# Performance work log

Measured on AMD Instinct MI355X. Metric: run time of the kernel, lower is better.

## Reference

```python
import jax, jax.numpy as jnp
import numpy as np

N_HEAD = 8
D_MODEL = 1024   # also the sequence length L (the code requires L == d_model)
D_K = 256
D_V = 256
D_TRANS = 256
B = 32
KS = 13
PAD = 6
LN_EPS = 1e-3
TEMPER = float(np.sqrt(D_MODEL))


def conv1d(x, w, b):
    # x: (B, Cin, L), w: (Cout, Cin, K) torch layout, 'same' padding 6
    y = jax.lax.conv_general_dilated(
        x, w, window_strides=(1,), padding=[(PAD, PAD)],
        dimension_numbers=('NCH', 'OIH', 'NCH'))
    return y + b[None, :, None]


def setup_inputs() -> dict:
    key = jax.random.key(0)
    ks = jax.random.split(key, 16)
    n = lambda i, shape, s=1.0: jax.random.normal(ks[i], shape, jnp.float32) * s
    return {
        'q': n(0, (B, D_K, D_MODEL)),
        'k': n(1, (B, D_K, D_MODEL)),
        'v': n(2, (B, D_V, D_MODEL)),
        'cq_w': n(3, (D_TRANS, D_K, KS), 0.02), 'cq_b': jnp.zeros((D_TRANS,), jnp.float32),
        'ck_w': n(4, (D_TRANS, D_K, KS), 0.02), 'ck_b': jnp.zeros((D_TRANS,), jnp.float32),
        'cv_w': n(5, (D_TRANS, D_V, KS), 0.02), 'cv_b': jnp.zeros((D_TRANS,), jnp.float32),
        'w_qs': n(6, (N_HEAD, D_MODEL, D_TRANS), 0.02),
        'w_ks': n(7, (N_HEAD, D_MODEL, D_TRANS), 0.02),
        'w_vs': n(8, (N_HEAD, D_MODEL, D_TRANS), 0.02),
        'proj_w': n(9, (D_MODEL, N_HEAD * D_TRANS), 0.02),
        'proj_b': jnp.zeros((D_MODEL,), jnp.float32),
        'fc_w': n(10, (D_V, D_TRANS, KS), 0.02), 'fc_b': jnp.zeros((D_V,), jnp.float32),
        'ln_a': jnp.ones((D_MODEL,), jnp.float32),
        'ln_b': jnp.zeros((D_MODEL,), jnp.float32),
    }


def reference(q, k, v, cq_w, cq_b, ck_w, ck_b, cv_w, cv_b,
              w_qs, w_ks, w_vs, proj_w, proj_b, fc_w, fc_b, ln_a, ln_b):
    # Conv1d QKV "projections": (B, d_k, L) -> (B, d_trans, L)
    q_b = conv1d(q, cq_w, cq_b)
    k_b = conv1d(k, ck_w, ck_b)
    v_b = conv1d(v, cv_w, cv_b)

    # Per-head projection along the L (==d_model) axis:
    # torch: (H, B*d_trans, L) bmm (H, L, d_trans) -> (H*B, d_trans, d_trans)
    q_s = jnp.einsum('btl,hld->hbtd', q_b, w_qs)  # (H, B, Dt, Dt)
    k_s = jnp.einsum('btl,hld->hbtd', k_b, w_ks)
    v_s = jnp.einsum('btl,hld->hbtd', v_b, w_vs)

    # Scaled dot-product attention over the d_trans axis (eval mode: dropout off)
    scores = jnp.einsum('hbqd,hbkd->hbqk', q_s, k_s) / TEMPER
    attn = jax.nn.softmax(scores, axis=-1)
    out = jnp.einsum('hbqk,hbkd->hbqd', attn, v_s)  # (H, B, Dt, Dt)

    # torch: split heads along batch dim, concat along last -> (B, Dt, H*Dt)
    outputs = out.transpose(1, 2, 0, 3).reshape(B, D_TRANS, N_HEAD * D_TRANS)
    outputs = outputs @ proj_w.T + proj_b            # (B, Dt, d_model)
    outputs = conv1d(outputs, fc_w, fc_b)            # (B, d_v, d_model)

    # Custom LayerNorm over last axis with unbiased std and eps added to sigma
    z = outputs + q
    mu = jnp.mean(z, axis=-1, keepdims=True)
    sigma = jnp.std(z, axis=-1, ddof=1, keepdims=True)
    output = (z - mu) / (sigma + LN_EPS) * ln_a + ln_b

    attns = attn.reshape(N_HEAD * B, D_TRANS, D_TRANS)
    return output, attns
```

## Files before the change

### kernel.cpp

```cpp
#include <hip/hip_runtime.h>

typedef unsigned short u16;
typedef __attribute__((ext_vector_type(8))) short short8;
typedef __attribute__((ext_vector_type(4))) float f32x4;

__device__ __forceinline__ float bf2f(u16 x) {
  unsigned u = ((unsigned)x) << 16;
  return __builtin_bit_cast(float, u);
}
__device__ __forceinline__ u16 f2bf(float x) {
  unsigned u = __builtin_bit_cast(unsigned, x);
  u += 0x7fffu + ((u >> 16) & 1u);
  return (u16)(u >> 16);
}

__device__ __forceinline__ void gl2lds16(const u16* g, u16* l) {
  __builtin_amdgcn_global_load_lds(
      (const __attribute__((address_space(1))) unsigned*)g,
      (__attribute__((address_space(3))) unsigned*)l, 16, 0, 0);
}

__global__ void detect_kernel(const void* ln_a, unsigned* flag) {
  if (threadIdx.x == 0 && blockIdx.x == 0)
    *flag = (*(const unsigned*)ln_a == 0x3F800000u) ? 1u : 0u;
}

#define GEMM_TILE(T, RB, DO_STAGE, SB, VMCNT, ENDBAR)                         \
  {                                                                           \
    const u16* ring_ = smem + (RB)*BUF;                                       \
    short8 af_[4], bq_[4];                                                    \
    _Pragma("unroll") for (int i_ = 0; i_ < 4; i_++)                          \
        af_[i_] = *(const short8*)(ring_ + offA[i_]);                         \
    _Pragma("unroll") for (int j_ = 0; j_ < 4; j_++)                          \
        bq_[j_] = *(const short8*)(ring_ + offB[j_]);                         \
    if (DO_STAGE) stage_tile((T) + AHEAD, (SB));                              \
    __builtin_amdgcn_s_barrier();                                             \
    asm volatile("s_waitcnt lgkmcnt(0)" ::: "memory");                        \
    __builtin_amdgcn_sched_barrier(0);                                        \
    __builtin_amdgcn_s_setprio(1);                                            \
    _Pragma("unroll") for (int i_ = 0; i_ < 4; i_++)                          \
        _Pragma("unroll") for (int j_ = 0; j_ < 4; j_++)                      \
            acc[i_][j_] = __builtin_amdgcn_mfma_f32_16x16x32_bf16(            \
                af_[i_], bq_[j_], acc[i_][j_], 0, 0, 0);                      \
    __builtin_amdgcn_s_setprio(0);                                            \
    if constexpr (WIDE) {                                                     \
      _Pragma("unroll") for (int i_ = 0; i_ < 4; i_++)                        \
          af_[i_] = *(const short8*)(ring_ + offA[4 + i_]);                   \
      asm volatile("s_waitcnt lgkmcnt(0)" ::: "memory");                      \
      __builtin_amdgcn_sched_barrier(0);                                      \
      __builtin_amdgcn_s_setprio(1);                                          \
      _Pragma("unroll") for (int i_ = 0; i_ < 4; i_++)                        \
          _Pragma("unroll") for (int j_ = 0; j_ < 4; j_++)                    \
              acc[4 + i_][j_] = __builtin_amdgcn_mfma_f32_16x16x32_bf16(      \
                  af_[i_], bq_[j_], acc[4 + i_][j_], 0, 0, 0);                \
      __builtin_amdgcn_s_setprio(0);                                          \
    }                                                                         \
    if ((VMCNT) == 6) asm volatile("s_waitcnt vmcnt(6)" ::: "memory");        \
    else if ((VMCNT) == 4) asm volatile("s_waitcnt vmcnt(4)" ::: "memory");   \
    else if ((VMCNT) == 3) asm volatile("s_waitcnt vmcnt(3)" ::: "memory");   \
    else if ((VMCNT) == 0) asm volatile("s_waitcnt vmcnt(0)" ::: "memory");   \
    if (ENDBAR) __builtin_amdgcn_s_barrier();                                 \
  }

template <typename OutT, bool WIDE>
__global__ __launch_bounds__(512, 2) void gemm_kernel(
    const u16* __restrict__ A, const u16* __restrict__ B, OutT* __restrict__ C,
    const u16* __restrict__ bias, int K, int lda, int ldb, int ldc,
    long a0, long a1, long a2, long b0, long b1, long b2,
    long c0, long c1, long c2, int biasMid, float alpha) {
  extern __shared__ u16 smem[];
  constexpr int BN = WIDE ? 256 : 128;
  constexpr int BUF = WIDE ? 16384 : 12288;
  constexpr int RING = WIDE ? 3 : 4;
  constexpr int AHEAD = RING - 1;
  constexpr int NCALL = WIDE ? 4 : 3;
  constexpr int MI = WIDE ? 8 : 4;

  const int tid = threadIdx.x;
  const int z = blockIdx.z;
  const int zlo = z & 31, zmid = (z >> 5) & 7, zhi = z >> 8;
  const u16* Ab = A + (long)zlo * a0 + (long)zmid * a1 + (long)zhi * a2;
  const u16* Bb = B + (long)zlo * b0 + (long)zmid * b1 + (long)zhi * b2;
  OutT* Cb = C + (long)zlo * c0 + (long)zmid * c1 + (long)zhi * c2;
  const int m0 = blockIdx.y * 256;
  const int n0 = blockIdx.x * BN;

  const int wave = tid >> 6;
  const int lane = tid & 63;

  const int lgrp = lane >> 3;
  const int slot = lane & 7;
  const u16* gsrc[NCALL];
  int ldsoff[NCALL];
#pragma unroll
  for (int c = 0; c < NCALL; c++) {
    const bool isA = (c < 2);
    const int L0 = (isA ? c : (c - 2)) * 64 + wave * 8;
    const int L = L0 + lgrp;
    const int ls = slot ^ (L & 7);
    const int row = 2 * L + (ls >> 2);
    const int blk = ls & 3;
    if (isA) {
      gsrc[c] = Ab + (long)(m0 + row) * lda + blk * 8;
      ldsoff[c] = L0 * 64;
    } else {
      gsrc[c] = Bb + (long)(n0 + row) * ldb + blk * 8;
      ldsoff[c] = 8192 + L0 * 64;
    }
  }

  auto stage_tile = [&](int t, int buf) {
    u16* dst = smem + buf * BUF;
    const long koff = (long)t * 32;
#pragma unroll
    for (int c = 0; c < NCALL; c++) gl2lds16(gsrc[c] + koff, dst + ldsoff[c]);
  };

  const int wm = WIDE ? ((wave >> 2) * 128) : ((wave >> 1) * 64);
  const int wn = WIDE ? ((wave & 3) * 64) : ((wave & 1) * 64);
  const int quad = lane >> 4;
  const int r = lane & 15;
  int offA[MI], offB[4];
#pragma unroll
  for (int i = 0; i < MI; i++) {
    const int rowA = wm + i * 16 + r;
    const int lnA = rowA >> 1;
    offA[i] = lnA * 64 + ((((rowA & 1) * 4 + quad) ^ (lnA & 7)) * 8);
  }
#pragma unroll
  for (int j = 0; j < 4; j++) {
    const int rowB = wn + j * 16 + r;
    const int lnB = rowB >> 1;
    offB[j] = 8192 + lnB * 64 + ((((rowB & 1) * 4 + quad) ^ (lnB & 7)) * 8);
  }

  f32x4 acc[MI][4] = {};
  const int nt = K >> 5;

#pragma unroll
  for (int i = 0; i < AHEAD; i++) stage_tile(i, i);
  if constexpr (WIDE)
    asm volatile("s_waitcnt vmcnt(4)" ::: "memory");
  else
    asm volatile("s_waitcnt vmcnt(6)" ::: "memory");
  __builtin_amdgcn_s_barrier();

  int t = 0, rbuf = 0, sbuf = AHEAD;
  for (; t < nt - AHEAD; ++t) {
    GEMM_TILE(t, rbuf, true, sbuf, (WIDE ? 4 : 6), true);
    rbuf = (rbuf + 1 == RING) ? 0 : rbuf + 1;
    sbuf = (sbuf + 1 == RING) ? 0 : sbuf + 1;
  }
  if constexpr (!WIDE) {
    GEMM_TILE(t, rbuf, false, 0, 3, true);
    ++t;
    rbuf = (rbuf + 1 == RING) ? 0 : rbuf + 1;
  }
  GEMM_TILE(t, rbuf, false, 0, 0, true);
  ++t;
  rbuf = (rbuf + 1 == RING) ? 0 : rbuf + 1;
  GEMM_TILE(t, rbuf, false, 0, -1, false);

  const u16* biasb = bias ? bias + (long)zmid * biasMid : nullptr;
#pragma unroll
  for (int i = 0; i < MI; i++) {
#pragma unroll
    for (int rr = 0; rr < 4; rr++) {
      const int mg = m0 + wm + i * 16 + quad * 4 + rr;
      const float bv = biasb ? bf2f(biasb[mg]) : 0.0f;
#pragma unroll
      for (int j = 0; j < 4; j++) {
        const int ng = n0 + wn + j * 16 + r;
        float val = acc[i][j][rr] * alpha + bv;
        if constexpr (__is_same(OutT, float))
          Cb[(long)mg * ldc + ng] = val;
        else
          Cb[(long)mg * ldc + ng] = f2bf(val);
      }
    }
  }
}

__global__ __launch_bounds__(256) void transpose_kernel(
    const void* __restrict__ i0, const void* __restrict__ i1,
    const void* __restrict__ i2, u16* __restrict__ out, int R, int C,
    long ostride, int ooff, int zdiv, const unsigned* __restrict__ flagp) {
  const bool f32 = *flagp != 0;
  __shared__ u16 t[64 * 68];
  const int z = blockIdx.z;
  const void* in = (z < zdiv) ? i0 : (z < 2 * zdiv) ? i1 : i2;
  const int zq = (z < zdiv) ? z : (z < 2 * zdiv) ? z - zdiv : z - 2 * zdiv;
  const long ibase = (long)zq * R * C;
  const int r0 = blockIdx.y * 64;
  const int c0 = blockIdx.x * 64;
  u16* ob = out + (long)z * ostride + ooff;
  const int tid = threadIdx.x;
#pragma unroll
  for (int i = 0; i < 4; i++) {
    const int vv = tid + i * 256;
    const int rr = vv >> 4;
    const int cc = (vv & 15) << 2;
    uint2 packed;
    if (f32) {
      const float4 fv = *(const float4*)((const float*)in + ibase +
                                         (long)(r0 + rr) * C + (c0 + cc));
      packed.x = (unsigned)f2bf(fv.x) | ((unsigned)f2bf(fv.y) << 16);
      packed.y = (unsigned)f2bf(fv.z) | ((unsigned)f2bf(fv.w) << 16);
    } else {
      packed = *(const uint2*)((const u16*)in + ibase + (long)(r0 + rr) * C +
                               (c0 + cc));
    }
    *(uint2*)(&t[rr * 68 + cc]) = packed;
  }
  __syncthreads();
#pragma unroll
  for (int i = 0; i < 4; i++) {
    const int vv = tid + i * 256;
    const int cc = vv >> 4;
    const int rr = (vv & 15) << 2;
    unsigned lo = (unsigned)t[rr * 68 + cc] | ((unsigned)t[(rr + 1) * 68 + cc] << 16);
    unsigned hi =
        (unsigned)t[(rr + 2) * 68 + cc] | ((unsigned)t[(rr + 3) * 68 + cc] << 16);
    uint2 val = {lo, hi};
    *(uint2*)(ob + (long)(c0 + cc) * R + (r0 + rr)) = val;
  }
}

__global__ __launch_bounds__(256) void pack_w_kernel(
    const void* __restrict__ w0, const void* __restrict__ w1,
    const void* __restrict__ w2, const void* __restrict__ w3,
    u16* __restrict__ out, const unsigned* __restrict__ flagp) {
  const bool f32 = *flagp != 0;
  const int y = blockIdx.y;
  const void* in = (y == 0) ? w0 : (y == 1) ? w1 : (y == 2) ? w2 : w3;
  u16* o = out + (long)y * 851968;
  const int t = blockIdx.x * 256 + threadIdx.x;
  const int co = t / 3328;
  const int rem = t - co * 3328;
  const int dk = rem >> 8;
  const int ci = rem & 255;
  const int src = co * 3328 + ci * 13 + dk;
  o[t] = f32 ? f2bf(((const float*)in)[src]) : ((const u16*)in)[src];
}

__global__ __launch_bounds__(256) void cvt_kernel(const void* __restrict__ in,
                                                  u16* __restrict__ out, long n,
                                                  const unsigned* __restrict__ flagp) {
  const bool f32 = *flagp != 0;
  const long i = ((long)blockIdx.x * 256 + threadIdx.x) * 8;
  if (i >= n) return;
  if (f32) {
    const float* p = (const float*)in + i;
    const float4 a = *(const float4*)p;
    const float4 b = *(const float4*)(p + 4);
    uint4 o;
    o.x = (unsigned)f2bf(a.x) | ((unsigned)f2bf(a.y) << 16);
    o.y = (unsigned)f2bf(a.z) | ((unsigned)f2bf(a.w) << 16);
    o.z = (unsigned)f2bf(b.x) | ((unsigned)f2bf(b.y) << 16);
    o.w = (unsigned)f2bf(b.z) | ((unsigned)f2bf(b.w) << 16);
    *(uint4*)(out + i) = o;
  } else {
    *(uint4*)(out + i) = *(const uint4*)((const u16*)in + i);
  }
}

__global__ __launch_bounds__(256) void bias_cvt_kernel(
    const void* __restrict__ s0, const void* __restrict__ s1,
    const void* __restrict__ s2, const void* __restrict__ s3,
    const void* __restrict__ s4, u16* __restrict__ out,
    const unsigned* __restrict__ flagp) {
  const bool f32 = *flagp != 0;
  const long i = threadIdx.x * 8;
  const void* src;
  long off;
  if (i < 256) { src = s0; off = i; }
  else if (i < 512) { src = s1; off = i - 256; }
  else if (i < 768) { src = s2; off = i - 512; }
  else if (i < 1024) { src = s3; off = i - 768; }
  else { src = s4; off = i - 1024; }
  if (f32) {
    const float* p = (const float*)src + off;
    const float4 a = *(const float4*)p;
    const float4 b = *(const float4*)(p + 4);
    uint4 o;
    o.x = (unsigned)f2bf(a.x) | ((unsigned)f2bf(a.y) << 16);
    o.y = (unsigned)f2bf(a.z) | ((unsigned)f2bf(a.w) << 16);
    o.z = (unsigned)f2bf(b.x) | ((unsigned)f2bf(b.y) << 16);
    o.w = (unsigned)f2bf(b.z) | ((unsigned)f2bf(b.w) << 16);
    *(uint4*)(out + i) = o;
  } else {
    *(uint4*)(out + i) = *(const uint4*)((const u16*)src + off);
  }
}

__global__ __launch_bounds__(256) void zeropad_kernel(u16* __restrict__ base,
                                                      long bstride, int nb) {
  const int t = blockIdx.x * 256 + threadIdx.x;
  if (t >= nb * 384) return;
  const int b = t / 384;
  const int rem = t - b * 384;
  const int rp = rem >> 5;
  const int col = (rem & 31) * 8;
  const int row = rp < 6 ? rp : 1024 + rp;
  uint4 zz = {0u, 0u, 0u, 0u};
  *(uint4*)(base + (long)b * bstride + row * 256 + col) = zz;
}

__global__ __launch_bounds__(256) void softmax_kernel(
    u16* __restrict__ sc, void* __restrict__ dout,
    const unsigned* __restrict__ flagp) {
  const bool f32 = *flagp != 0;
  const long row = (long)blockIdx.x * 4 + (threadIdx.x >> 6);
  const int lane = threadIdx.x & 63;
  const uint2 raw = *(const uint2*)(sc + row * 256 + lane * 4);
  float s0 = bf2f((u16)(raw.x & 0xffff)), s1 = bf2f((u16)(raw.x >> 16));
  float s2 = bf2f((u16)(raw.y & 0xffff)), s3 = bf2f((u16)(raw.y >> 16));
  float m = fmaxf(fmaxf(s0, s1), fmaxf(s2, s3));
  for (int o = 32; o > 0; o >>= 1) m = fmaxf(m, __shfl_xor(m, o, 64));
  float e0 = expf(s0 - m), e1 = expf(s1 - m), e2 = expf(s2 - m), e3 = expf(s3 - m);
  float sum = e0 + e1 + e2 + e3;
  for (int o = 32; o > 0; o >>= 1) sum += __shfl_xor(sum, o, 64);
  const float inv = 1.0f / sum;
  const float p0 = e0 * inv, p1 = e1 * inv, p2 = e2 * inv, p3 = e3 * inv;
  uint2 ov;
  ov.x = (unsigned)f2bf(p0) | ((unsigned)f2bf(p1) << 16);
  ov.y = (unsigned)f2bf(p2) | ((unsigned)f2bf(p3) << 16);
  *(uint2*)(sc + row * 256 + lane * 4) = ov;
  if (f32) {
    float4 o4 = {p0, p1, p2, p3};
    *(float4*)((float*)dout + 8388608 + row * 256 + lane * 4) = o4;
  } else {
    *(uint2*)((u16*)dout + 8388608 + row * 256 + lane * 4) = ov;
  }
}

__global__ __launch_bounds__(256) void ln_kernel(
    const float* __restrict__ fc, const void* __restrict__ qraw,
    const void* __restrict__ la, const void* __restrict__ lb,
    void* __restrict__ dout, const unsigned* __restrict__ flagp) {
  const bool f32 = *flagp != 0;
  __shared__ float red[4];
  const long row = blockIdx.x;
  const int tid = threadIdx.x;
  const int col = tid * 4;
  const float4 zf = *(const float4*)(fc + row * 1024 + col);
  float q0, q1, q2, q3;
  if (f32) {
    const float4 t = *(const float4*)((const float*)qraw + row * 1024 + col);
    q0 = t.x; q1 = t.y; q2 = t.z; q3 = t.w;
  } else {
    const uint2 qr = *(const uint2*)((const u16*)qraw + row * 1024 + col);
    q0 = bf2f((u16)(qr.x & 0xffff)); q1 = bf2f((u16)(qr.x >> 16));
    q2 = bf2f((u16)(qr.y & 0xffff)); q3 = bf2f((u16)(qr.y >> 16));
  }
  const float z0 = zf.x + q0, z1 = zf.y + q1, z2 = zf.z + q2, z3 = zf.w + q3;
  float s = z0 + z1 + z2 + z3;
  for (int o = 32; o > 0; o >>= 1) s += __shfl_xor(s, o, 64);
  if ((tid & 63) == 0) red[tid >> 6] = s;
  __syncthreads();
  const float mu = (red[0] + red[1] + red[2] + red[3]) * (1.0f / 1024.0f);
  __syncthreads();
  const float d0 = z0 - mu, d1 = z1 - mu, d2 = z2 - mu, d3 = z3 - mu;
  float ss = d0 * d0 + d1 * d1 + d2 * d2 + d3 * d3;
  for (int o = 32; o > 0; o >>= 1) ss += __shfl_xor(ss, o, 64);
  if ((tid & 63) == 0) red[tid >> 6] = ss;
  __syncthreads();
  const float var = (red[0] + red[1] + red[2] + red[3]) * (1.0f / 1023.0f);
  const float inv = 1.0f / (sqrtf(var) + 1e-3f);
  float a0, a1, a2, a3, b0, b1, b2, b3;
  if (f32) {
    const float4 ta = *(const float4*)((const float*)la + col);
    const float4 tb = *(const float4*)((const float*)lb + col);
    a0 = ta.x; a1 = ta.y; a2 = ta.z; a3 = ta.w;
    b0 = tb.x; b1 = tb.y; b2 = tb.z; b3 = tb.w;
  } else {
    const uint2 ta = *(const uint2*)((const u16*)la + col);
    const uint2 tb = *(const uint2*)((const u16*)lb + col);
    a0 = bf2f((u16)(ta.x & 0xffff)); a1 = bf2f((u16)(ta.x >> 16));
    a2 = bf2f((u16)(ta.y & 0xffff)); a3 = bf2f((u16)(ta.y >> 16));
    b0 = bf2f((u16)(tb.x & 0xffff)); b1 = bf2f((u16)(tb.x >> 16));
    b2 = bf2f((u16)(tb.y & 0xffff)); b3 = bf2f((u16)(tb.y >> 16));
  }
  const float o0 = d0 * inv * a0 + b0, o1 = d1 * inv * a1 + b1;
  const float o2v = d2 * inv * a2 + b2, o3 = d3 * inv * a3 + b3;
  if (f32) {
    float4 o4 = {o0, o1, o2v, o3};
    *(float4*)((float*)dout + row * 1024 + col) = o4;
  } else {
    uint2 o2;
    o2.x = (unsigned)f2bf(o0) | ((unsigned)f2bf(o1) << 16);
    o2.y = (unsigned)f2bf(o2v) | ((unsigned)f2bf(o3) << 16);
    *(uint2*)((u16*)dout + row * 1024 + col) = o2;
  }
}

enum : long {
  OWPQ = 0,
  OWPK = 851968,
  OWPV = 1703936,
  OWPFC = 2555904,
  OWQT = 3407872,
  OWKT = 5505024,
  OWVT = 7602176,
  OPW16 = 9699328,
  OBQKV = 11796480,
  OBFC = 11797248,
  OBPROJ = 11797504,
  OFLAG = 11798528,
  OQB = 11798536,
  OKB = 20187144,
  OVB = 28575752,
  OQS = 36964360,
  OKS = 53741576,
  OVST = 70518792,
  OXPAD = OQS,
  OSC = OQB,
  OOUTC = OQS,
  OPROJP = OKS,
  OFC = OVST,
};

extern "C" void kernel_launch(void* const* d_in, const int* in_sizes, int n_in,
                              void* d_out, int out_size, void* d_ws,
                              size_t ws_size, hipStream_t stream) {
  const void* q = d_in[0];
  const void* k = d_in[1];
  const void* v = d_in[2];
  const void* cq_w = d_in[3];
  const void* cq_b = d_in[4];
  const void* ck_w = d_in[5];
  const void* ck_b = d_in[6];
  const void* cv_w = d_in[7];
  const void* cv_b = d_in[8];
  const void* w_qs = d_in[9];
  const void* w_ks = d_in[10];
  const void* w_vs = d_in[11];
  const void* proj_w = d_in[12];
  const void* proj_b = d_in[13];
  const void* fc_w = d_in[14];
  const void* fc_b = d_in[15];
  const void* ln_a = d_in[16];
  const void* ln_b = d_in[17];

  u16* ws = (u16*)d_ws;
  unsigned* flag = (unsigned*)(ws + OFLAG);

  static int attr_done = 0;
  if (!attr_done) {
    hipFuncSetAttribute(reinterpret_cast<const void*>(&gemm_kernel<u16, true>),
                        hipFuncAttributeMaxDynamicSharedMemorySize, 98304);
    hipFuncSetAttribute(reinterpret_cast<const void*>(&gemm_kernel<u16, false>),
                        hipFuncAttributeMaxDynamicSharedMemorySize, 98304);
    hipFuncSetAttribute(reinterpret_cast<const void*>(&gemm_kernel<float, false>),
                        hipFuncAttributeMaxDynamicSharedMemorySize, 98304);
    attr_done = 1;
  }

  detect_kernel<<<1, 64, 0, stream>>>(ln_a, flag);

  pack_w_kernel<<<dim3(3328, 4), 256, 0, stream>>>(cq_w, ck_w, cv_w, fc_w,
                                                   ws + OWPQ, flag);
  transpose_kernel<<<dim3(4, 16, 24), 256, 0, stream>>>(
      w_qs, w_ks, w_vs, ws + OWQT, 1024, 256, 262144, 0, 8, flag);
  cvt_kernel<<<1024, 256, 0, stream>>>(proj_w, ws + OPW16, 2097152, flag);
  bias_cvt_kernel<<<1, 256, 0, stream>>>(cq_b, ck_b, cv_b, fc_b, proj_b,
                                         ws + OBQKV, flag);

  zeropad_kernel<<<144, 256, 0, stream>>>(ws + OXPAD, 265216, 96);
  transpose_kernel<<<dim3(16, 4, 96), 256, 0, stream>>>(
      q, k, v, ws + OXPAD, 256, 1024, 265216, 1536, 32, flag);

  gemm_kernel<u16, true><<<dim3(4, 1, 96), 512, 98304, stream>>>(
      ws + OWPQ, ws + OXPAD, ws + OQB, ws + OBQKV, 3328, 3328, 256, 1024,
      0, 851968, 0, 265216, 8486912, 0, 262144, 8388608, 0, 256, 1.0f);

  gemm_kernel<u16, true><<<dim3(1, 1, 512), 512, 98304, stream>>>(
      ws + OQB, ws + OWQT, ws + OQS, nullptr, 1024, 1024, 1024, 256,
      262144, 0, 8388608, 0, 262144, 2097152, 65536, 2097152, 16777216, 0, 1.0f);
  gemm_kernel<u16, true><<<dim3(1, 1, 256), 512, 98304, stream>>>(
      ws + OWVT, ws + OVB, ws + OVST, nullptr, 1024, 1024, 1024, 256,
      0, 262144, 0, 262144, 0, 0, 65536, 2097152, 0, 0, 1.0f);

  gemm_kernel<u16, true><<<dim3(1, 1, 256), 512, 98304, stream>>>(
      ws + OQS, ws + OKS, ws + OSC, nullptr, 256, 256, 256, 256,
      65536, 2097152, 0, 65536, 2097152, 0, 65536, 2097152, 0, 0, 0.03125f);

  softmax_kernel<<<16384, 256, 0, stream>>>(ws + OSC, d_out, flag);

  gemm_kernel<u16, true><<<dim3(1, 1, 256), 512, 98304, stream>>>(
      ws + OSC, ws + OVST, ws + OOUTC, nullptr, 256, 256, 256, 2048,
      65536, 2097152, 0, 65536, 2097152, 0, 524288, 256, 0, 0, 1.0f);

  zeropad_kernel<<<48, 256, 0, stream>>>(ws + OPROJP, 265216, 32);
  gemm_kernel<u16, false><<<dim3(2, 4, 32), 512, 98304, stream>>>(
      ws + OPW16, ws + OOUTC, ws + OPROJP + 1536, ws + OBPROJ, 2048, 2048, 2048,
      256, 0, 0, 0, 524288, 0, 0, 265216, 0, 0, 0, 1.0f);

  gemm_kernel<float, false><<<dim3(8, 1, 32), 512, 98304, stream>>>(
      ws + OWPFC, ws + OPROJP, (float*)(ws + OFC), ws + OBFC, 3328, 3328, 256,
      1024, 0, 0, 0, 265216, 0, 0, 262144, 0, 0, 0, 1.0f);

  ln_kernel<<<8192, 256, 0, stream>>>((const float*)(ws + OFC), q, ln_a, ln_b,
                                      d_out, flag);

  (void)in_sizes; (void)n_in; (void)out_size; (void)ws_size;
}
```

Measured before the change: 794.2 us.

## Restructure GEMM main loop into split-A register prefetch with three-buffer ring

Replaces the macro-based GEMM tile loop with a single loop that keeps a fixed three-buffer LDS ring, prefetching the next tile's A-low and B fragments into registers while MFMAs on the current half run. Each iteration uses one barrier plus staged lgkmcnt waits, so LDS reads overlap compute more finely. The conv QKV GEMM also switches from the wide 256-column tile to the narrow 128-column tile, doubling the grid to raise occupancy. Risks: more register pressure, a full vmcnt(0) wait every iteration, and the narrow variant now uses only 3 of its 4 ring buffers with a different vmcnt count.

```diff
diff --git a/kernel.cpp b/kernel.cpp
--- a/kernel.cpp
+++ b/kernel.cpp
@@ -24,43 +24,6 @@
   if (threadIdx.x == 0 && blockIdx.x == 0)
     *flag = (*(const unsigned*)ln_a == 0x3F800000u) ? 1u : 0u;
 }
-
-#define GEMM_TILE(T, RB, DO_STAGE, SB, VMCNT, ENDBAR)                         \
-  {                                                                           \
-    const u16* ring_ = smem + (RB)*BUF;                                       \
-    short8 af_[4], bq_[4];                                                    \
-    _Pragma("unroll") for (int i_ = 0; i_ < 4; i_++)                          \
-        af_[i_] = *(const short8*)(ring_ + offA[i_]);                         \
-    _Pragma("unroll") for (int j_ = 0; j_ < 4; j_++)                          \
-        bq_[j_] = *(const short8*)(ring_ + offB[j_]);                         \
-    if (DO_STAGE) stage_tile((T) + AHEAD, (SB));                              \
-    __builtin_amdgcn_s_barrier();                                             \
-    asm volatile("s_waitcnt lgkmcnt(0)" ::: "memory");                        \
-    __builtin_amdgcn_sched_barrier(0);                                        \
-    __builtin_amdgcn_s_setprio(1);                                            \
-    _Pragma("unroll") for (int i_ = 0; i_ < 4; i_++)                          \
-        _Pragma("unroll") for (int j_ = 0; j_ < 4; j_++)                      \
-            acc[i_][j_] = __builtin_amdgcn_mfma_f32_16x16x32_bf16(            \
-                af_[i_], bq_[j_], acc[i_][j_], 0, 0, 0);                      \
-    __builtin_amdgcn_s_setprio(0);                                            \
-    if constexpr (WIDE) {                                                     \
-      _Pragma("unroll") for (int i_ = 0; i_ < 4; i_++)                        \
-          af_[i_] = *(const short8*)(ring_ + offA[4 + i_]);                   \
-      asm volatile("s_waitcnt lgkmcnt(0)" ::: "memory");                      \
-      __builtin_amdgcn_sched_barrier(0);                                      \
-      __builtin_amdgcn_s_setprio(1);                                          \
-      _Pragma("unroll") for (int i_ = 0; i_ < 4; i_++)                        \
-          _Pragma("unroll") for (int j_ = 0; j_ < 4; j_++)                    \
-              acc[4 + i_][j_] = __builtin_amdgcn_mfma_f32_16x16x32_bf16(      \
-                  af_[i_], bq_[j_], acc[4 + i_][j_], 0, 0, 0);                \
-      __builtin_amdgcn_s_setprio(0);                                          \
-    }                                                                         \
-    if ((VMCNT) == 6) asm volatile("s_waitcnt vmcnt(6)" ::: "memory");        \
-    else if ((VMCNT) == 4) asm volatile("s_waitcnt vmcnt(4)" ::: "memory");   \
-    else if ((VMCNT) == 3) asm volatile("s_waitcnt vmcnt(3)" ::: "memory");   \
-    else if ((VMCNT) == 0) asm volatile("s_waitcnt vmcnt(0)" ::: "memory");   \
-    if (ENDBAR) __builtin_amdgcn_s_barrier();                                 \
-  }
 
 template <typename OutT, bool WIDE>
 __global__ __launch_bounds__(512, 2) void gemm_kernel(
@@ -71,10 +34,9 @@
   extern __shared__ u16 smem[];
   constexpr int BN = WIDE ? 256 : 128;
   constexpr int BUF = WIDE ? 16384 : 12288;
-  constexpr int RING = WIDE ? 3 : 4;
-  constexpr int AHEAD = RING - 1;
   constexpr int NCALL = WIDE ? 4 : 3;
   constexpr int MI = WIDE ? 8 : 4;
+  constexpr int H = MI / 2;
 
   const int tid = threadIdx.x;
   const int z = blockIdx.z;
@@ -135,31 +97,82 @@
   }
 
   f32x4 acc[MI][4] = {};
+  short8 aLo[H], aHi[H], bq[4];
   const int nt = K >> 5;
 
-#pragma unroll
-  for (int i = 0; i < AHEAD; i++) stage_tile(i, i);
+  stage_tile(0, 0);
+  stage_tile(1, 1);
   if constexpr (WIDE)
     asm volatile("s_waitcnt vmcnt(4)" ::: "memory");
   else
-    asm volatile("s_waitcnt vmcnt(6)" ::: "memory");
+    asm volatile("s_waitcnt vmcnt(3)" ::: "memory");
   __builtin_amdgcn_s_barrier();
-
-  int t = 0, rbuf = 0, sbuf = AHEAD;
-  for (; t < nt - AHEAD; ++t) {
-    GEMM_TILE(t, rbuf, true, sbuf, (WIDE ? 4 : 6), true);
-    rbuf = (rbuf + 1 == RING) ? 0 : rbuf + 1;
-    sbuf = (sbuf + 1 == RING) ? 0 : sbuf + 1;
-  }
-  if constexpr (!WIDE) {
-    GEMM_TILE(t, rbuf, false, 0, 3, true);
-    ++t;
-    rbuf = (rbuf + 1 == RING) ? 0 : rbuf + 1;
-  }
-  GEMM_TILE(t, rbuf, false, 0, 0, true);
-  ++t;
-  rbuf = (rbuf + 1 == RING) ? 0 : rbuf + 1;
-  GEMM_TILE(t, rbuf, false, 0, -1, false);
+  __builtin_amdgcn_sched_barrier(0);
+#pragma unroll
+  for (int i = 0; i < H; i++) aLo[i] = *(const short8*)(smem + offA[i]);
+#pragma unroll
+  for (int j = 0; j < 4; j++) bq[j] = *(const short8*)(smem + offB[j]);
+  __builtin_amdgcn_sched_barrier(0);
+
+  int rb = 0;
+  for (int t = 0; t < nt; ++t) {
+    const int rb1 = (rb == 2) ? 0 : rb + 1;
+    const int rb2 = (rb1 == 2) ? 0 : rb1 + 1;
+    const u16* base0 = smem + rb * BUF;
+    const u16* base1 = smem + rb1 * BUF;
+    const bool hasN = (t + 1 < nt);
+    if (hasN) {
+      asm volatile("s_waitcnt vmcnt(0)" ::: "memory");
+      __builtin_amdgcn_s_barrier();
+      __builtin_amdgcn_sched_barrier(0);
+      if (t + 2 < nt) stage_tile(t + 2, rb2);
+      __builtin_amdgcn_sched_barrier(0);
+    }
+#pragma unroll
+    for (int i = 0; i < H; i++) aHi[i] = *(const short8*)(base0 + offA[H + i]);
+    __builtin_amdgcn_sched_barrier(0);
+    if constexpr (WIDE)
+      asm volatile("s_waitcnt lgkmcnt(4)" ::: "memory");
+    else
+      asm volatile("s_waitcnt lgkmcnt(2)" ::: "memory");
+    __builtin_amdgcn_sched_barrier(0);
+    __builtin_amdgcn_s_setprio(1);
+#pragma unroll
+    for (int i = 0; i < H; i++)
+#pragma unroll
+      for (int j = 0; j < 4; j++)
+        acc[i][j] =
+            __builtin_amdgcn_mfma_f32_16x16x32_bf16(aLo[i], bq[j], acc[i][j], 0, 0, 0);
+    __builtin_amdgcn_s_setprio(0);
+    if (hasN) {
+#pragma unroll
+      for (int i = 0; i < H; i++) aLo[i] = *(const short8*)(base1 + offA[i]);
+    }
+    __builtin_amdgcn_sched_barrier(0);
+    if (hasN) {
+      if constexpr (WIDE)
+        asm volatile("s_waitcnt lgkmcnt(4)" ::: "memory");
+      else
+        asm volatile("s_waitcnt lgkmcnt(2)" ::: "memory");
+    } else {
+      asm volatile("s_waitcnt lgkmcnt(0)" ::: "memory");
+    }
+    __builtin_amdgcn_sched_barrier(0);
+    __builtin_amdgcn_s_setprio(1);
+#pragma unroll
+    for (int i = 0; i < H; i++)
+#pragma unroll
+      for (int j = 0; j < 4; j++)
+        acc[H + i][j] = __builtin_amdgcn_mfma_f32_16x16x32_bf16(aHi[i], bq[j],
+                                                                acc[H + i][j], 0, 0, 0);
+    __builtin_amdgcn_s_setprio(0);
+    if (hasN) {
+#pragma unroll
+      for (int j = 0; j < 4; j++) bq[j] = *(const short8*)(base1 + offB[j]);
+      __builtin_amdgcn_sched_barrier(0);
+    }
+    rb = rb1;
+  }
 
   const u16* biasb = bias ? bias + (long)zmid * biasMid : nullptr;
 #pragma unroll
@@ -470,7 +483,7 @@
   transpose_kernel<<<dim3(16, 4, 96), 256, 0, stream>>>(
       q, k, v, ws + OXPAD, 256, 1024, 265216, 1536, 32, flag);
 
-  gemm_kernel<u16, true><<<dim3(4, 1, 96), 512, 98304, stream>>>(
+  gemm_kernel<u16, false><<<dim3(8, 1, 96), 512, 98304, stream>>>(
       ws + OWPQ, ws + OXPAD, ws + OQB, ws + OBQKV, 3328, 3328, 256, 1024,
       0, 851968, 0, 265216, 8486912, 0, 262144, 8388608, 0, 256, 1.0f);
 
```

Result: slower. 842.3 us (+6.1%).
